# Kernel optimization log

Measured on AMD Instinct MI355X. Metric: run time of the kernel, lower is better.

Reference implementation:

```python
import jax, jax.numpy as jnp
import numpy as np

N_FEATURES = 60
WINDOW = 64
N_FFT_BINS = WINDOW // 2 + 1  # 33
HIDDEN = 256
N_OUT = 3
TOTAL_IN = N_FEATURES + N_FEATURES * N_FFT_BINS  # 2040


def setup_inputs() -> dict:
    key = jax.random.key(0)
    ks = jax.random.split(key, 9)
    B, T = 4, 4096
    x = jax.random.normal(ks[0], (B, T, N_FEATURES), dtype=jnp.float32)

    def lin(k, fan_in, fan_out):
        bound = 1.0 / np.sqrt(fan_in)
        kw, kb = jax.random.split(k)
        W = jax.random.uniform(kw, (fan_in, fan_out), minval=-bound, maxval=bound, dtype=jnp.float32)
        b = jax.random.uniform(kb, (fan_out,), minval=-bound, maxval=bound, dtype=jnp.float32)
        return W, b

    W1, b1 = lin(ks[1], TOTAL_IN, HIDDEN)
    W2, b2 = lin(ks[2], HIDDEN, HIDDEN)
    W3, b3 = lin(ks[3], HIDDEN, HIDDEN // 2)
    W4, b4 = lin(ks[4], HIDDEN // 2, N_OUT)
    return {"x": x, "W1": W1, "b1": b1, "W2": W2, "b2": b2,
            "W3": W3, "b3": b3, "W4": W4, "b4": b4}


def _fft_features(x):
    # x: [B, T, F]
    B, T, F = x.shape
    half_w = WINDOW // 2
    # reflect pad along time: (half_w, half_w - 1)
    xp = jnp.pad(x, ((0, 0), (half_w, half_w - 1), (0, 0)), mode='reflect')  # [B, T+W-1, F]
    # sliding windows: [B, T, W, F] -> [B, T, F, W] (matches torch unfold layout)
    idx = jnp.arange(T)[:, None] + jnp.arange(WINDOW)[None, :]  # [T, W]
    windows = xp[:, idx, :].transpose(0, 1, 3, 2)  # [B, T, F, W]
    fft_mag = jnp.log1p(jnp.abs(jnp.fft.rfft(windows, axis=-1)))  # [B, T, F, W//2+1]
    return fft_mag.reshape(B, T, F * N_FFT_BINS)


def reference(x, W1, b1, W2, b2, W3, b3, W4, b4):
    fft_flat = _fft_features(x)
    h = jnp.concatenate([x, fft_flat], axis=-1)  # [B, T, 2040]
    h = jax.nn.relu(h @ W1 + b1)   # dropout is identity in eval mode
    h = jax.nn.relu(h @ W2 + b2)
    h = jax.nn.relu(h @ W3 + b3)
    return h @ W4 + b4             # [B, T, 3]
```

## Files before the change

### kernel.cpp

```cpp
#include <hip/hip_runtime.h>
#include <math.h>

#define T_LEN 4096
#define NF 60
#define NBINS 33
#define KPAD 2048
#define HID 256
#define NTOK 16384
#define LINE 4208

typedef _Float16 half_t;
typedef half_t half8 __attribute__((ext_vector_type(8)));
typedef half_t half4 __attribute__((ext_vector_type(4)));
typedef float f32x4 __attribute__((ext_vector_type(4)));

constexpr double K_PI = 3.14159265358979323846;
constexpr double tcos(double x) {
    while (x >  K_PI) x -= 2.0 * K_PI;
    while (x < -K_PI) x += 2.0 * K_PI;
    double x2 = x * x, s = 0.0, term = 1.0;
    for (int m = 0; m < 14; ++m) { s += term; term *= -x2 / ((2.0*m + 1.0) * (2.0*m + 2.0)); }
    return s;
}
struct CosTab { float v[64]; };
constexpr CosTab make_tab() {
    CosTab t{};
    for (int j = 0; j < 64; ++j) t.v[j] = (float)tcos(2.0 * K_PI * (double)j / 64.0);
    return t;
}
__device__ constexpr CosTab CTd = make_tab();

__device__ __forceinline__ float log2_1p(float x) {
    return __log2f(1.0f + x);
}

__global__ __launch_bounds__(256) void prep_kernel(
        const float* __restrict__ W1, const float* __restrict__ W2,
        const float* __restrict__ W3,
        half_t* __restrict__ dftH,
        half_t* __restrict__ W1T, half_t* __restrict__ W2T,
        half_t* __restrict__ W3T) {
    int i = blockIdx.x * 256 + threadIdx.x;
    if (i < 4096) {
        int row = i >> 6, n = i & 63;
        float c = (row < 33) ? CTd.v[(row * n) & 63]
                             : CTd.v[((row - 32) * n + 48) & 63];
        dftH[i] = (half_t)c;
        return;
    }
    i -= 4096;
    if (i < 256 * KPAD) {
        int gk = i & (KPAD - 1);
        float v = 0.f;
        if (gk < 2040) {
            int j = i >> 11;
            int r;
            bool isfft = true;
            if (gk < 1920) {
                int f = gk >> 5, bin = gk & 31;
                r = NF + f * NBINS + bin;
            } else if (gk < 1980) {
                r = gk - 1920; isfft = false;
            } else {
                r = NF + (gk - 1980) * NBINS + 32;
            }
            v = W1[(size_t)r * HID + j];
            if (isfft) v *= 0.69314718055994531f;
        }
        W1T[i] = (half_t)v;
        return;
    }
    i -= 256 * KPAD;
    if (i < 256 * 256) {
        int k = i & 255, j = i >> 8;
        W2T[i] = (half_t)W2[(size_t)k * HID + j];
        return;
    }
    i -= 256 * 256;
    if (i < 128 * 256) {
        int k = i & 255, j = i >> 8;
        W3T[i] = (half_t)W3[(size_t)k * 128 + j];
    }
}

__global__ __launch_bounds__(256) void xline_kernel(
        const float* __restrict__ x, half_t* __restrict__ lineG) {
    const int bf = blockIdx.x;
    const int b = bf / NF, f = bf - b * NF;
    const float* xb = x + (size_t)b * T_LEN * NF + f;
    half_t* L = lineG + (size_t)bf * LINE;
    for (int j = threadIdx.x; j < LINE; j += 256) {
        int s = j - 32;
        int r = (s < 0) ? -s : ((s > T_LEN - 1) ? 2 * (T_LEN - 1) - s : s);
        L[j] = (half_t)xb[(size_t)r * NF];
    }
}

__global__ __launch_bounds__(256) void raw_kernel(
        const float* __restrict__ x, half_t* __restrict__ H0) {
    const int t = blockIdx.x * 256 + threadIdx.x;
    const int b = t >> 12, tl = t & (T_LEN - 1);
    const int i = (b << 12) + ((tl & 7) << 9) + (tl >> 3);
    const float* xp = x + (size_t)t * NF;
    half_t* hp = H0 + (size_t)i * KPAD;
#pragma unroll
    for (int f4 = 0; f4 < 15; ++f4) {
        float4 v = *(const float4*)(xp + f4 * 4);
        half4 h;
        h[0] = (half_t)v.x; h[1] = (half_t)v.y;
        h[2] = (half_t)v.z; h[3] = (half_t)v.w;
        *(half4*)&hp[1920 + f4 * 4] = h;
    }
    half8 z = {};
    *(half8*)&hp[2040] = z;
}

__global__ __launch_bounds__(256) void fft_hankel(
        const half_t* __restrict__ lineG, const half_t* __restrict__ dftH,
        half_t* __restrict__ H0) {
    __shared__ half_t L[2176];

    const int bid = blockIdx.x;
    const int bf = bid >> 4, c = (bid >> 1) & 7, hf = bid & 1;
    const int b = bf / NF, f = bf - b * NF;
    const int tid = threadIdx.x;
    const int lane = tid & 63, wv = tid >> 6;
    const int lr = lane & 15, lg = lane >> 4;

    half8 a[4][2];
#pragma unroll
    for (int rf = 0; rf < 4; ++rf)
#pragma unroll
        for (int ks = 0; ks < 2; ++ks)
            a[rf][ks] = *(const half8*)&dftH[(16 * rf + lr) * 64 + ks * 32 + lg * 8];

    {
        const half_t* src = lineG + (size_t)bf * LINE + hf * 2048 + c;
        for (int j = tid; j < 2144; j += 256) L[j] = src[j];
    }
    __syncthreads();

    const int i0 = (b << 12) + (c << 9) + (hf << 8);

#pragma unroll
    for (int cs = 0; cs < 4; ++cs) {
        const int s0 = wv * 64 + cs * 16;
        half8 w0 = *(const half8*)&L[8 * (s0 + lr) + lg * 8];
        half8 w1 = *(const half8*)&L[8 * (s0 + lr) + 32 + lg * 8];
        f32x4 dacc[4] = {};
#pragma unroll
        for (int rf = 0; rf < 4; ++rf)
            dacc[rf] = __builtin_amdgcn_mfma_f32_16x16x32_f16(a[rf][0], w0, dacc[rf], 0, 0, 0);
#pragma unroll
        for (int rf = 0; rf < 4; ++rf)
            dacc[rf] = __builtin_amdgcn_mfma_f32_16x16x32_f16(a[rf][1], w1, dacc[rf], 0, 0, 0);

        half_t* base = H0 + (size_t)(i0 + s0 + lr) * KPAD;
#pragma unroll
        for (int rf = 0; rf < 2; ++rf) {
            half4 h4;
#pragma unroll
            for (int r = 0; r < 4; ++r) {
                float re = dacc[rf][r];
                float im = dacc[rf + 2][r];
                float v = (rf == 0 && r == 0)
                    ? ((lg == 0) ? log2_1p(fabsf(re))
                                 : log2_1p(sqrtf(re * re + im * im)))
                    : log2_1p(sqrtf(re * re + im * im));
                h4[r] = (half_t)v;
            }
            *(half4*)&base[f * 32 + 16 * rf + 4 * lg] = h4;
        }
        if (lg == 0)
            base[1980 + f] = (half_t)log2_1p(fabsf(dacc[2][0]));
    }
}

template<int BM, int BN, bool OUT_F32>
__global__ __launch_bounds__(256, 2) void gemm_f16(
        const half_t* __restrict__ A, int lda,
        const half_t* __restrict__ BT, int ldb,
        const float* __restrict__ bias,
        half_t* __restrict__ Ch, float* __restrict__ Cf,
        int N, int K) {
    constexpr int MFR = BM / 16;
    constexpr int NFR = BN / 64;
    constexpr int BUNITS = BN * 8 / 256;
    __shared__ half_t As[BM][72];
    __shared__ half_t Bs[BN][72];

    const int tid  = threadIdx.x;
    const int row0 = blockIdx.x * BM;
    const int col0 = blockIdx.y * BN;
    const int wv = tid >> 6, lane = tid & 63;
    const int lr = lane & 15, lg = lane >> 4;

    f32x4 acc[MFR][NFR] = {};

    for (int k0 = 0; k0 < K; k0 += 64) {
        half8 av0, av1;
        if (BM == 64) {
            const int arow = tid >> 2, ak = (tid & 3) * 16;
            const half_t* ap = A + (size_t)(row0 + arow) * lda + ak + k0;
            av0 = *(const half8*)ap;
            av1 = *(const half8*)(ap + 8);
        } else {
            const int arow = tid >> 3, ak = (tid & 7) * 8;
            av0 = *(const half8*)(A + (size_t)(row0 + arow) * lda + ak + k0);
        }
        half8 bv[BUNITS];
#pragma unroll
        for (int u = 0; u < BUNITS; ++u) {
            int e = tid + u * 256;
            int n = e >> 3, c8 = (e & 7) * 8;
            bv[u] = *(const half8*)(BT + (size_t)(col0 + n) * ldb + k0 + c8);
        }

        __syncthreads();

        if (BM == 64) {
            const int arow = tid >> 2, ak = (tid & 3) * 16;
            *(half8*)&As[arow][ak]     = av0;
            *(half8*)&As[arow][ak + 8] = av1;
        } else {
            const int arow = tid >> 3, ak = (tid & 7) * 8;
            *(half8*)&As[arow][ak] = av0;
        }
#pragma unroll
        for (int u = 0; u < BUNITS; ++u) {
            int e = tid + u * 256;
            int n = e >> 3, c8 = (e & 7) * 8;
            *(half8*)&Bs[n][c8] = bv[u];
        }

        __syncthreads();

#pragma unroll
        for (int ks = 0; ks < 2; ++ks) {
            half8 af[MFR], bf[NFR];
#pragma unroll
            for (int mf = 0; mf < MFR; ++mf)
                af[mf] = *(const half8*)&As[mf * 16 + lr][ks * 32 + lg * 8];
#pragma unroll
            for (int nf = 0; nf < NFR; ++nf)
                bf[nf] = *(const half8*)&Bs[wv * (16 * NFR) + nf * 16 + lr][ks * 32 + lg * 8];
#pragma unroll
            for (int mf = 0; mf < MFR; ++mf)
#pragma unroll
                for (int nf = 0; nf < NFR; ++nf)
                    acc[mf][nf] = __builtin_amdgcn_mfma_f32_16x16x32_f16(af[mf], bf[nf], acc[mf][nf], 0, 0, 0);
        }
    }

#pragma unroll
    for (int nf = 0; nf < NFR; ++nf) {
        int col = col0 + wv * (16 * NFR) + nf * 16 + lr;
        float bs = bias[col];
#pragma unroll
        for (int mf = 0; mf < MFR; ++mf)
#pragma unroll
            for (int r = 0; r < 4; ++r) {
                int row = row0 + mf * 16 + lg * 4 + r;
                float v = fmaxf(acc[mf][nf][r] + bs, 0.f);
                if (OUT_F32) Cf[(size_t)row * N + col] = v;
                else         Ch[(size_t)row * N + col] = (half_t)v;
            }
    }
}

__global__ __launch_bounds__(256) void head_kernel(
        const float* __restrict__ H, const float* __restrict__ W4,
        const float* __restrict__ b4, float* __restrict__ out) {
    __shared__ float Ws[128 * 3];
    __shared__ float bs[3];
    for (int i = threadIdx.x; i < 384; i += 256) Ws[i] = W4[i];
    if (threadIdx.x < 3) bs[threadIdx.x] = b4[threadIdx.x];
    __syncthreads();
    const int i = blockIdx.x * 256 + threadIdx.x;
    const float* h = H + (size_t)i * 128;
    float a0 = bs[0], a1 = bs[1], a2 = bs[2];
#pragma unroll
    for (int k = 0; k < 128; ++k) {
        float hv = h[k];
        a0 = fmaf(hv, Ws[k * 3 + 0], a0);
        a1 = fmaf(hv, Ws[k * 3 + 1], a1);
        a2 = fmaf(hv, Ws[k * 3 + 2], a2);
    }
    const int b = i >> 12, c = (i >> 9) & 7, s = i & 511;
    const int t = (b << 12) + (s << 3) + c;
    float* o = out + (size_t)t * 3;
    o[0] = a0; o[1] = a1; o[2] = a2;
}

extern "C" void kernel_launch(void* const* d_in, const int* in_sizes, int n_in,
                              void* d_out, int out_size, void* d_ws, size_t ws_size,
                              hipStream_t stream) {
    (void)in_sizes; (void)n_in; (void)out_size; (void)ws_size;
    const float* x  = (const float*)d_in[0];
    const float* W1 = (const float*)d_in[1];
    const float* b1 = (const float*)d_in[2];
    const float* W2 = (const float*)d_in[3];
    const float* b2 = (const float*)d_in[4];
    const float* W3 = (const float*)d_in[5];
    const float* b3 = (const float*)d_in[6];
    const float* W4 = (const float*)d_in[7];
    const float* b4 = (const float*)d_in[8];
    float* out = (float*)d_out;

    char* w = (char*)d_ws;
    half_t* H0    = (half_t*)(w);
    half_t* H1    = (half_t*)(w + (size_t)64 * 1024 * 1024);
    half_t* H2    = (half_t*)(w + (size_t)72 * 1024 * 1024);
    float*  H3    = (float*) (w + (size_t)80 * 1024 * 1024);
    half_t* W1T   = (half_t*)(w + (size_t)88 * 1024 * 1024);
    half_t* W2T   = (half_t*)(w + (size_t)89 * 1024 * 1024);
    half_t* W3T   = W2T + 256 * 256;
    half_t* dftH  = W3T + 128 * 256;
    half_t* lineG = (half_t*)(w + (size_t)90 * 1024 * 1024);

    prep_kernel<<<2448, 256, 0, stream>>>(W1, W2, W3, dftH, W1T, W2T, W3T);
    xline_kernel<<<240, 256, 0, stream>>>(x, lineG);
    raw_kernel<<<NTOK / 256, 256, 0, stream>>>(x, H0);
    fft_hankel<<<240 * 16, 256, 0, stream>>>(lineG, dftH, H0);

    gemm_f16<32, 128, false><<<dim3(NTOK / 32, 2), 256, 0, stream>>>(
        H0, KPAD, W1T, KPAD, b1, H1, nullptr, HID, KPAD);
    gemm_f16<64, 128, false><<<dim3(NTOK / 64, 2), 256, 0, stream>>>(
        H1, HID, W2T, HID, b2, H2, nullptr, HID, HID);
    gemm_f16<64, 64, true><<<dim3(NTOK / 64, 2), 256, 0, stream>>>(
        H2, HID, W3T, HID, b3, nullptr, H3, HID / 2, HID);

    head_kernel<<<NTOK / 256, 256, 0, stream>>>(H3, W4, b4, out);
}
```

Baseline: 119.9 us.

## Load GEMM B fragments directly from global and double-buffer A tile in LDS

```diff
diff --git a/kernel.cpp b/kernel.cpp
--- a/kernel.cpp
+++ b/kernel.cpp
@@ -176,79 +176,64 @@
     }
 }
 
-template<int BM, int BN, bool OUT_F32>
-__global__ __launch_bounds__(256, 2) void gemm_f16(
+template<int BN, bool OUT_F32>
+__global__ __launch_bounds__(256, 2) void gemm_bdir(
         const half_t* __restrict__ A, int lda,
         const half_t* __restrict__ BT, int ldb,
         const float* __restrict__ bias,
         half_t* __restrict__ Ch, float* __restrict__ Cf,
         int N, int K) {
-    constexpr int MFR = BM / 16;
     constexpr int NFR = BN / 64;
-    constexpr int BUNITS = BN * 8 / 256;
-    __shared__ half_t As[BM][72];
-    __shared__ half_t Bs[BN][72];
+    __shared__ half_t As[2][64][72];
 
     const int tid  = threadIdx.x;
-    const int row0 = blockIdx.x * BM;
+    const int row0 = blockIdx.x * 64;
     const int col0 = blockIdx.y * BN;
     const int wv = tid >> 6, lane = tid & 63;
     const int lr = lane & 15, lg = lane >> 4;
 
-    f32x4 acc[MFR][NFR] = {};
-
-    for (int k0 = 0; k0 < K; k0 += 64) {
+    const int arow = tid >> 2, ak = (tid & 3) * 16;
+    const half_t* ap = A + (size_t)(row0 + arow) * lda + ak;
+
+    f32x4 acc[4][NFR] = {};
+    const int NIT = K / 64;
+
+    {
+        half8 v0 = *(const half8*)(ap);
+        half8 v1 = *(const half8*)(ap + 8);
+        *(half8*)&As[0][arow][ak]     = v0;
+        *(half8*)&As[0][arow][ak + 8] = v1;
+    }
+
+    for (int it = 0; it < NIT; ++it) {
+        const int cur = it & 1;
         half8 av0, av1;
-        if (BM == 64) {
-            const int arow = tid >> 2, ak = (tid & 3) * 16;
-            const half_t* ap = A + (size_t)(row0 + arow) * lda + ak + k0;
-            av0 = *(const half8*)ap;
-            av1 = *(const half8*)(ap + 8);
-        } else {
-            const int arow = tid >> 3, ak = (tid & 7) * 8;
-            av0 = *(const half8*)(A + (size_t)(row0 + arow) * lda + ak + k0);
-        }
-        half8 bv[BUNITS];
-#pragma unroll
-        for (int u = 0; u < BUNITS; ++u) {
-            int e = tid + u * 256;
-            int n = e >> 3, c8 = (e & 7) * 8;
-            bv[u] = *(const half8*)(BT + (size_t)(col0 + n) * ldb + k0 + c8);
-        }
-
+        if (it + 1 < NIT) {
+            av0 = *(const half8*)(ap + (it + 1) * 64);
+            av1 = *(const half8*)(ap + (it + 1) * 64 + 8);
+        }
         __syncthreads();
-
-        if (BM == 64) {
-            const int arow = tid >> 2, ak = (tid & 3) * 16;
-            *(half8*)&As[arow][ak]     = av0;
-            *(half8*)&As[arow][ak + 8] = av1;
-        } else {
-            const int arow = tid >> 3, ak = (tid & 7) * 8;
-            *(half8*)&As[arow][ak] = av0;
-        }
-#pragma unroll
-        for (int u = 0; u < BUNITS; ++u) {
-            int e = tid + u * 256;
-            int n = e >> 3, c8 = (e & 7) * 8;
-            *(half8*)&Bs[n][c8] = bv[u];
-        }
-
-        __syncthreads();
-
+        const int k0 = it * 64;
 #pragma unroll
         for (int ks = 0; ks < 2; ++ks) {
-            half8 af[MFR], bf[NFR];
-#pragma unroll
-            for (int mf = 0; mf < MFR; ++mf)
-                af[mf] = *(const half8*)&As[mf * 16 + lr][ks * 32 + lg * 8];
-#pragma unroll
-            for (int nf = 0; nf < NFR; ++nf)
-                bf[nf] = *(const half8*)&Bs[wv * (16 * NFR) + nf * 16 + lr][ks * 32 + lg * 8];
-#pragma unroll
-            for (int mf = 0; mf < MFR; ++mf)
+            half8 af[4], bf[NFR];
+#pragma unroll
+            for (int mf = 0; mf < 4; ++mf)
+                af[mf] = *(const half8*)&As[cur][mf * 16 + lr][ks * 32 + lg * 8];
+#pragma unroll
+            for (int nf = 0; nf < NFR; ++nf) {
+                int col = col0 + wv * (16 * NFR) + nf * 16 + lr;
+                bf[nf] = *(const half8*)&BT[(size_t)col * ldb + k0 + ks * 32 + lg * 8];
+            }
+#pragma unroll
+            for (int mf = 0; mf < 4; ++mf)
 #pragma unroll
                 for (int nf = 0; nf < NFR; ++nf)
                     acc[mf][nf] = __builtin_amdgcn_mfma_f32_16x16x32_f16(af[mf], bf[nf], acc[mf][nf], 0, 0, 0);
+        }
+        if (it + 1 < NIT) {
+            *(half8*)&As[cur ^ 1][arow][ak]     = av0;
+            *(half8*)&As[cur ^ 1][arow][ak + 8] = av1;
         }
     }
 
@@ -257,7 +242,7 @@
         int col = col0 + wv * (16 * NFR) + nf * 16 + lr;
         float bs = bias[col];
 #pragma unroll
-        for (int mf = 0; mf < MFR; ++mf)
+        for (int mf = 0; mf < 4; ++mf)
 #pragma unroll
             for (int r = 0; r < 4; ++r) {
                 int row = row0 + mf * 16 + lg * 4 + r;
@@ -323,11 +308,11 @@
     raw_kernel<<<NTOK / 256, 256, 0, stream>>>(x, H0);
     fft_hankel<<<240 * 16, 256, 0, stream>>>(lineG, dftH, H0);
 
-    gemm_f16<32, 128, false><<<dim3(NTOK / 32, 2), 256, 0, stream>>>(
+    gemm_bdir<128, false><<<dim3(NTOK / 64, 2), 256, 0, stream>>>(
         H0, KPAD, W1T, KPAD, b1, H1, nullptr, HID, KPAD);
-    gemm_f16<64, 128, false><<<dim3(NTOK / 64, 2), 256, 0, stream>>>(
+    gemm_bdir<128, false><<<dim3(NTOK / 64, 2), 256, 0, stream>>>(
         H1, HID, W2T, HID, b2, H2, nullptr, HID, HID);
-    gemm_f16<64, 64, true><<<dim3(NTOK / 64, 2), 256, 0, stream>>>(
+    gemm_bdir<64, true><<<dim3(NTOK / 64, 2), 256, 0, stream>>>(
         H2, HID, W3T, HID, b3, nullptr, H3, HID / 2, HID);
 
     head_kernel<<<NTOK / 256, 256, 0, stream>>>(H3, W4, b4, out);
```

Result: slower. 125.1 us (+4.3%).
